# Kernel tuning notes

Measured on AMD Instinct MI355X. Metric: run time of the kernel, lower is better.

## Reference

```python
import jax, jax.numpy as jnp
import numpy as np

N_NODES = 100000
N_EDGES = 1600000
D_IN = 128
D_HID = 128
D_OUT = 40


def _linear_init(key, fan_in, fan_out):
    # torch nn.Linear default: U(-1/sqrt(fan_in), 1/sqrt(fan_in)) for W and b
    kw, kb = jax.random.split(key)
    bound = 1.0 / np.sqrt(fan_in)
    W = jax.random.uniform(kw, (fan_in, fan_out), jnp.float32, -bound, bound)
    b = jax.random.uniform(kb, (fan_out,), jnp.float32, -bound, bound)
    return W, b


def setup_inputs() -> dict:
    key = jax.random.key(0)
    ks = jax.random.split(key, 8)
    x = jax.random.normal(ks[0], (N_NODES, D_IN), jnp.float32)
    edges = jax.random.randint(ks[1], (2, N_EDGES), 0, N_NODES, jnp.int64)
    # layer 0: MLP(128 -> 128 -> 128)
    W1_0, b1_0 = _linear_init(ks[2], D_IN, D_HID)
    W2_0, b2_0 = _linear_init(ks[3], D_HID, D_HID)
    # layer 1: MLP(128 -> 128 -> 128)
    W1_1, b1_1 = _linear_init(ks[4], D_HID, D_HID)
    W2_1, b2_1 = _linear_init(ks[5], D_HID, D_HID)
    # layer 2: MLP(128 -> 128 -> 40)
    W1_2, b1_2 = _linear_init(ks[6], D_HID, D_HID)
    W2_2, b2_2 = _linear_init(ks[7], D_HID, D_OUT)
    eps = jnp.zeros(())  # GINConv train_eps=True initializes eps=0
    return {
        "x": x, "edges": edges,
        "W1_0": W1_0, "b1_0": b1_0, "W2_0": W2_0, "b2_0": b2_0, "eps_0": eps,
        "W1_1": W1_1, "b1_1": b1_1, "W2_1": W2_1, "b2_1": b2_1, "eps_1": eps,
        "W1_2": W1_2, "b1_2": b1_2, "W2_2": W2_2, "b2_2": b2_2, "eps_2": eps,
    }


def _gin_conv(x, src, dst, eps, W1, b1, W2, b2):
    # sum-aggregate neighbor features: out_i = MLP((1+eps)*x_i + sum_{j->i} x_j)
    aggr = jax.ops.segment_sum(x[src], dst, num_segments=x.shape[0])
    h = (1.0 + eps) * x + aggr
    h = jnp.maximum(h @ W1 + b1, 0.0)  # MLP layer 1 + ReLU
    return h @ W2 + b2                  # MLP layer 2


def reference(x, edges,
              W1_0, b1_0, W2_0, b2_0, eps_0,
              W1_1, b1_1, W2_1, b2_1, eps_1,
              W1_2, b1_2, W2_2, b2_2, eps_2):
    src, dst = edges[0], edges[1]
    # dropout is identity at inference (training=False)
    h = jax.nn.relu(_gin_conv(x, src, dst, eps_0, W1_0, b1_0, W2_0, b2_0))
    h = jax.nn.relu(_gin_conv(h, src, dst, eps_1, W1_1, b1_1, W2_1, b2_1))
    o = _gin_conv(h, src, dst, eps_2, W1_2, b1_2, W2_2, b2_2)
    return jax.nn.log_softmax(o, axis=1)
```

## Files before the change

kernel.cpp:

```cpp
#include <hip/hip_runtime.h>
#include <stdint.h>

typedef __attribute__((ext_vector_type(8))) short short8;
typedef __attribute__((ext_vector_type(4))) short short4v;
typedef __attribute__((ext_vector_type(4))) float float4v;

__device__ __forceinline__ float bf2f(unsigned short s) {
    union { unsigned int u; float f; } c; c.u = ((unsigned int)s) << 16; return c.f;
}
__device__ __forceinline__ unsigned short f2bf(float f) {
    union { float f; unsigned int u; } c; c.f = f;
    unsigned int x = c.u;
    unsigned int r = x + 0x7fffu + ((x >> 16) & 1u);
    return (unsigned short)(r >> 16);
}
__device__ __forceinline__ void unpack2(unsigned int u, float& lo, float& hi) {
    union { unsigned int uu; float ff; } a, b;
    a.uu = u << 16;
    b.uu = u & 0xffff0000u;
    lo = a.ff; hi = b.ff;
}

__global__ __launch_bounds__(256) void bs_count(const int* __restrict__ dst, int nE,
                                                int* __restrict__ bucketCnt) {
    __shared__ int c[512];
    int t = threadIdx.x;
    for (int i = t; i < 512; i += 256) c[i] = 0;
    __syncthreads();
    int base = blockIdx.x * 4096;
    for (int i = t; i < 4096; i += 256) {
        int e = base + i;
        if (e < nE) atomicAdd(&c[dst[e] >> 8], 1);
    }
    __syncthreads();
    for (int i = t; i < 512; i += 256)
        if (c[i]) atomicAdd(&bucketCnt[i], c[i]);
}

__global__ __launch_bounds__(512) void bs_scan(const int* __restrict__ bucketCnt,
                                               int* __restrict__ bucketBase,
                                               int* __restrict__ bucketCur,
                                               int* __restrict__ off, int M, int nE) {
    __shared__ int s[512];
    int t = threadIdx.x;
    int v = bucketCnt[t];
    s[t] = v;
    __syncthreads();
    for (int o = 1; o < 512; o <<= 1) {
        int x = (t >= o) ? s[t - o] : 0;
        __syncthreads();
        s[t] += x;
        __syncthreads();
    }
    bucketBase[t] = s[t] - v;
    bucketCur[t] = s[t] - v;
    if (t == 511) bucketBase[512] = s[511];
    if (t == 0) off[M] = nE;
}

__global__ __launch_bounds__(512) void bs_scatter(const int* __restrict__ src,
                                                  const int* __restrict__ dst, int nE,
                                                  int* __restrict__ bucketCur,
                                                  unsigned int* __restrict__ ebuf) {
    __shared__ int cnt[512];
    __shared__ int excl[512];
    __shared__ int chunk[512];
    __shared__ unsigned int buf[4096];
    __shared__ unsigned short bkt[4096];
    int t = threadIdx.x;
    cnt[t] = 0;
    __syncthreads();
    int base = blockIdx.x * 4096;
    int n = nE - base; if (n > 4096) n = 4096;
    unsigned int pk[8]; int bk[8]; int rk[8];
#pragma unroll
    for (int u = 0; u < 8; ++u) {
        int i = t + u * 512;
        if (i < n) {
            int e = base + i;
            int d = dst[e];
            int b = d >> 8;
            bk[u] = b;
            pk[u] = (unsigned int)src[e] | ((unsigned int)(d & 255) << 17);
            rk[u] = atomicAdd(&cnt[b], 1);
        } else bk[u] = -1;
    }
    __syncthreads();
    excl[t] = cnt[t];
    __syncthreads();
    for (int o = 1; o < 512; o <<= 1) {
        int x = (t >= o) ? excl[t - o] : 0;
        __syncthreads();
        excl[t] += x;
        __syncthreads();
    }
    int ex = excl[t] - cnt[t];
    __syncthreads();
    excl[t] = ex;
    if (cnt[t]) chunk[t] = atomicAdd(&bucketCur[t], cnt[t]);
    __syncthreads();
#pragma unroll
    for (int u = 0; u < 8; ++u) {
        if (bk[u] >= 0) {
            int lp = excl[bk[u]] + rk[u];
            buf[lp] = pk[u];
            bkt[lp] = (unsigned short)bk[u];
        }
    }
    __syncthreads();
    for (int i = t; i < n; i += 512) {
        int b = bkt[i];
        ebuf[chunk[b] + (i - excl[b])] = buf[i];
    }
}

__global__ __launch_bounds__(512) void bs_build(const unsigned int* __restrict__ ebuf,
                                                const int* __restrict__ bucketBase,
                                                int* __restrict__ off,
                                                int* __restrict__ esrc, int M) {
    __shared__ int cnt[256];
    __shared__ int excl[256];
    __shared__ int obuf[5120];
    int t = threadIdx.x, b = blockIdx.x;
    int base = bucketBase[b];
    int n = bucketBase[b + 1] - base;
    if (t < 256) cnt[t] = 0;
    __syncthreads();
    unsigned int pk[10]; int dl[10]; int rk[10];
#pragma unroll
    for (int u = 0; u < 10; ++u) {
        int i = t + u * 512;
        if (i < n) {
            unsigned int p = ebuf[base + i];
            pk[u] = p;
            int d = (p >> 17) & 255;
            dl[u] = d;
            rk[u] = atomicAdd(&cnt[d], 1);
        } else dl[u] = -1;
    }
    __syncthreads();
    if (t < 256) excl[t] = cnt[t];
    __syncthreads();
    for (int o = 1; o < 256; o <<= 1) {
        int x = (t < 256 && t >= o) ? excl[t - o] : 0;
        __syncthreads();
        if (t < 256) excl[t] += x;
        __syncthreads();
    }
    if (t < 256) {
        int ex = excl[t] - cnt[t];
        int node = b * 256 + t;
        if (node < M) off[node] = base + ex;
        excl[t] = ex;
    }
    __syncthreads();
#pragma unroll
    for (int u = 0; u < 10; ++u) {
        if (dl[u] >= 0) {
            int lp = excl[dl[u]] + rk[u];
            if (lp < 5120) obuf[lp] = (int)(pk[u] & 0x1FFFF);
        }
    }
    __syncthreads();
    for (int i = t; i < n; i += 512) esrc[base + i] = obuf[i];
}

struct Prep {
    const float* W[6];
    unsigned short* hi[6];
    const float4* xin;
    uint2* xout;
    int n4;
};

__global__ __launch_bounds__(256) void k_prep(Prep p) {
    int b = blockIdx.x;
    if (b < 344) {
        int mat = b >> 6;
        int rel = b - mat * 64;
        int NPAD = (mat == 5) ? 48 : 128;
        int N = (mat == 5) ? 40 : 128;
        int idx = rel * 256 + threadIdx.x;
        if (idx >= NPAD * 128) return;
        int n = idx >> 7, k = idx & 127;
        float w = (n < N) ? p.W[mat][k * N + n] : 0.f;
        p.hi[mat][idx] = f2bf(w);
    } else {
        int i = (b - 344) * 256 + threadIdx.x;
        if (i >= p.n4) return;
        float4 v = p.xin[i];
        uint2 o;
        o.x = ((unsigned int)f2bf(v.y) << 16) | f2bf(v.x);
        o.y = ((unsigned int)f2bf(v.w) << 16) | f2bf(v.z);
        p.xout[i] = o;
    }
}

__device__ __forceinline__ void acc8(uint4 v, float* s) {
    float a, b;
    unpack2(v.x, a, b); s[0] += a; s[1] += b;
    unpack2(v.y, a, b); s[2] += a; s[3] += b;
    unpack2(v.z, a, b); s[4] += a; s[5] += b;
    unpack2(v.w, a, b); s[6] += a; s[7] += b;
}

__global__ __launch_bounds__(256) void k_aggr(const uint4* __restrict__ Hin,
                                              const int* __restrict__ off,
                                              const int* __restrict__ esrc,
                                              const float* __restrict__ epsp,
                                              uint4* __restrict__ Ahi, int M) {
    int w = threadIdx.x >> 6, lane = threadIdx.x & 63;
    int li = lane & 15, q = lane >> 4;
    int node = blockIdx.x * 16 + w * 4 + q;
    if (node >= M) return;
    float ep = 1.0f + epsp[0];
    uint4 ow = Hin[node * 16 + li];
    float s[8] = {0.f, 0.f, 0.f, 0.f, 0.f, 0.f, 0.f, 0.f};
    int i = off[node], e = off[node + 1];
    for (; i + 8 <= e; i += 8) {
        uint4 v[8];
#pragma unroll
        for (int j = 0; j < 8; ++j) v[j] = Hin[esrc[i + j] * 16 + li];
#pragma unroll
        for (int j = 0; j < 8; ++j) acc8(v[j], s);
    }
    if (i < e) {
        int last = e - 1;
        uint4 v[8];
#pragma unroll
        for (int j = 0; j < 8; ++j) {
            int idx = i + j;
            int cl = idx < last ? idx : last;
            v[j] = Hin[esrc[cl] * 16 + li];
        }
#pragma unroll
        for (int j = 0; j < 8; ++j) {
            bool ok = (i + j) < e;
            uint4 u;
            u.x = ok ? v[j].x : 0u;
            u.y = ok ? v[j].y : 0u;
            u.z = ok ? v[j].z : 0u;
            u.w = ok ? v[j].w : 0u;
            acc8(u, s);
        }
    }
    float o[8];
    unpack2(ow.x, o[0], o[1]);
    unpack2(ow.y, o[2], o[3]);
    unpack2(ow.z, o[4], o[5]);
    unpack2(ow.w, o[6], o[7]);
#pragma unroll
    for (int k = 0; k < 8; ++k) s[k] = ep * o[k] + s[k];
    uint4 r;
    r.x = ((unsigned int)f2bf(s[1]) << 16) | f2bf(s[0]);
    r.y = ((unsigned int)f2bf(s[3]) << 16) | f2bf(s[2]);
    r.z = ((unsigned int)f2bf(s[5]) << 16) | f2bf(s[4]);
    r.w = ((unsigned int)f2bf(s[7]) << 16) | f2bf(s[6]);
    Ahi[node * 16 + li] = r;
}

template <int NT2, bool LOGITS>
__global__ __launch_bounds__(256, 4) void k_mlp(const unsigned short* __restrict__ AhiS,
                                                const unsigned short* __restrict__ W1h,
                                                const float* __restrict__ B1,
                                                const unsigned short* __restrict__ W2h,
                                                const float* __restrict__ B2,
                                                unsigned short* __restrict__ HOut,
                                                float* __restrict__ LOut, int M) {
    __shared__ short wbuf[128 * 136];
    int t = threadIdx.x, w = t >> 6, lane = t & 63;
    int lm = lane & 15, lg = lane >> 4;
    int rbase = blockIdx.x * 128;

    for (int i = t * 8; i < 128 * 128; i += 2048) {
        int n = i >> 7, k = i & 127;
        *(short8*)&wbuf[n * 136 + k] = *(const short8*)(W1h + i);
    }
    __syncthreads();

    short4v h2[2][8];
    bool act[2];
#pragma unroll
    for (int t2 = 0; t2 < 2; ++t2) {
        int r0 = rbase + t2 * 64 + w * 16;
        act[t2] = (r0 < M);
        if (act[t2]) {
            const short* Xp = (const short*)AhiS + (r0 + lm) * 128 + lg * 8;
            short8 xf[4];
#pragma unroll
            for (int kb = 0; kb < 4; ++kb) xf[kb] = *(const short8*)(Xp + kb * 32);
            float4v acc1[8];
#pragma unroll
            for (int nt = 0; nt < 8; ++nt) acc1[nt] = (float4v){0.f, 0.f, 0.f, 0.f};
#pragma unroll
            for (int nt = 0; nt < 8; ++nt) {
#pragma unroll
                for (int kb = 0; kb < 4; ++kb) {
                    short8 wf = *(const short8*)&wbuf[(nt * 16 + lm) * 136 + kb * 32 + lg * 8];
                    acc1[nt] = __builtin_amdgcn_mfma_f32_16x16x32_bf16(wf, xf[kb], acc1[nt], 0, 0, 0);
                }
            }
#pragma unroll
            for (int nt = 0; nt < 8; ++nt) {
                float4 b1 = *(const float4*)(B1 + nt * 16 + lg * 4);
                float v0 = acc1[nt][0] + b1.x; v0 = v0 > 0.f ? v0 : 0.f;
                float v1 = acc1[nt][1] + b1.y; v1 = v1 > 0.f ? v1 : 0.f;
                float v2 = acc1[nt][2] + b1.z; v2 = v2 > 0.f ? v2 : 0.f;
                float v3 = acc1[nt][3] + b1.w; v3 = v3 > 0.f ? v3 : 0.f;
                h2[t2][nt] = (short4v){(short)f2bf(v0), (short)f2bf(v1),
                                       (short)f2bf(v2), (short)f2bf(v3)};
            }
        } else {
#pragma unroll
            for (int nt = 0; nt < 8; ++nt) h2[t2][nt] = (short4v){0, 0, 0, 0};
        }
    }

    __syncthreads();
    for (int i = t * 8; i < NT2 * 16 * 128; i += 2048) {
        int n = i >> 7, k = i & 127;
        *(short8*)&wbuf[n * 136 + k] = *(const short8*)(W2h + i);
    }
    __syncthreads();

    float4v acc2[2][NT2];
#pragma unroll
    for (int t2 = 0; t2 < 2; ++t2)
#pragma unroll
        for (int ot = 0; ot < NT2; ++ot) acc2[t2][ot] = (float4v){0.f, 0.f, 0.f, 0.f};
#pragma unroll
    for (int ot = 0; ot < NT2; ++ot) {
#pragma unroll
        for (int nt = 0; nt < 8; ++nt) {
            short4v wf = *(const short4v*)&wbuf[(ot * 16 + lm) * 136 + nt * 16 + lg * 4];
#pragma unroll
            for (int t2 = 0; t2 < 2; ++t2)
                acc2[t2][ot] = __builtin_amdgcn_mfma_f32_16x16x16bf16_1k(wf, h2[t2][nt],
                                                                         acc2[t2][ot], 0, 0, 0);
        }
    }

#pragma unroll
    for (int t2 = 0; t2 < 2; ++t2) {
        if (!act[t2]) continue;
        int row = rbase + t2 * 64 + w * 16 + lm;
        if (!LOGITS) {
#pragma unroll
            for (int ot = 0; ot < NT2; ++ot) {
                float4 b2 = *(const float4*)(B2 + ot * 16 + lg * 4);
                float v0 = acc2[t2][ot][0] + b2.x; v0 = v0 > 0.f ? v0 : 0.f;
                float v1 = acc2[t2][ot][1] + b2.y; v1 = v1 > 0.f ? v1 : 0.f;
                float v2 = acc2[t2][ot][2] + b2.z; v2 = v2 > 0.f ? v2 : 0.f;
                float v3 = acc2[t2][ot][3] + b2.w; v3 = v3 > 0.f ? v3 : 0.f;
                uint2 pk;
                pk.x = ((unsigned int)f2bf(v1) << 16) | f2bf(v0);
                pk.y = ((unsigned int)f2bf(v3) << 16) | f2bf(v2);
                *(uint2*)(HOut + row * 128 + ot * 16 + lg * 4) = pk;
            }
        } else {
            float vv[NT2][4];
#pragma unroll
            for (int ot = 0; ot < NT2; ++ot) {
                int ub = ot * 16 + lg * 4;
                bool valid = ub <= 36;
                float4 b2 = valid ? *(const float4*)(B2 + ub) : (float4){0.f, 0.f, 0.f, 0.f};
                vv[ot][0] = valid ? acc2[t2][ot][0] + b2.x : -1e30f;
                vv[ot][1] = valid ? acc2[t2][ot][1] + b2.y : -1e30f;
                vv[ot][2] = valid ? acc2[t2][ot][2] + b2.z : -1e30f;
                vv[ot][3] = valid ? acc2[t2][ot][3] + b2.w : -1e30f;
            }
            float m = -1e30f;
#pragma unroll
            for (int ot = 0; ot < NT2; ++ot)
#pragma unroll
                for (int r = 0; r < 4; ++r) m = fmaxf(m, vv[ot][r]);
            m = fmaxf(m, __shfl_xor(m, 16, 64));
            m = fmaxf(m, __shfl_xor(m, 32, 64));
            float s = 0.f;
#pragma unroll
            for (int ot = 0; ot < NT2; ++ot)
#pragma unroll
                for (int r = 0; r < 4; ++r)
                    s += (vv[ot][r] > -1e29f) ? expf(vv[ot][r] - m) : 0.f;
            s += __shfl_xor(s, 16, 64);
            s += __shfl_xor(s, 32, 64);
            float ls = m + logf(s);
#pragma unroll
            for (int ot = 0; ot < NT2; ++ot) {
                int ub = ot * 16 + lg * 4;
                if (ub <= 36) {
                    float4 outv = {vv[ot][0] - ls, vv[ot][1] - ls,
                                   vv[ot][2] - ls, vv[ot][3] - ls};
                    *(float4*)(LOut + row * 40 + ub) = outv;
                }
            }
        }
    }
}

extern "C" void kernel_launch(void* const* d_in, const int* in_sizes, int n_in,
                              void* d_out, int out_size, void* d_ws, size_t ws_size,
                              hipStream_t stream) {
    const float* x    = (const float*)d_in[0];
    const int*   edges = (const int*)d_in[1];
    const float* eps0 = (const float*)d_in[6];
    const float* eps1 = (const float*)d_in[11];
    const float* eps2 = (const float*)d_in[16];
    const float* B1[3] = {(const float*)d_in[3], (const float*)d_in[8], (const float*)d_in[13]};
    const float* B2[3] = {(const float*)d_in[5], (const float*)d_in[10], (const float*)d_in[15]};

    int M  = in_sizes[0] / 128;
    int nE = in_sizes[1] / 2;
    const int* e_src = edges;
    const int* e_dst = edges + nE;

    char* ws = (char*)d_ws;
    size_t o = 0;
    auto alloc = [&](size_t bytes) {
        size_t p = o;
        o = (o + bytes + 511) & ~(size_t)511;
        return ws + p;
    };
    int* bucketCnt  = (int*)alloc(512 * 4);
    int* bucketBase = (int*)alloc(513 * 4);
    int* bucketCur  = (int*)alloc(512 * 4);
    int* off  = (int*)alloc((size_t)(M + 1) * 4);
    int* esrc = (int*)alloc((size_t)nE * 4);
    unsigned int* ebuf = (unsigned int*)alloc((size_t)nE * 4);

    Prep pp;
    pp.W[0] = (const float*)d_in[2];  pp.W[1] = (const float*)d_in[4];
    pp.W[2] = (const float*)d_in[7];  pp.W[3] = (const float*)d_in[9];
    pp.W[4] = (const float*)d_in[12]; pp.W[5] = (const float*)d_in[14];
    for (int m = 0; m < 6; ++m) {
        int npad = (m == 5) ? 48 : 128;
        pp.hi[m] = (unsigned short*)alloc((size_t)npad * 128 * 2);
    }
    unsigned short* xb  = (unsigned short*)alloc((size_t)M * 128 * 2);
    unsigned short* Ahi = (unsigned short*)alloc((size_t)M * 128 * 2);
    unsigned short* Hb  = (unsigned short*)alloc((size_t)M * 128 * 2);
    pp.xin = (const float4*)x;
    pp.xout = (uint2*)xb;
    pp.n4 = M * 32;
    (void)ws_size; (void)n_in; (void)out_size;

    hipMemsetAsync(bucketCnt, 0, 512 * 4, stream);
    int nChunk = (nE + 4095) / 4096;
    int nBk = (M + 255) / 256;
    bs_count<<<nChunk, 256, 0, stream>>>(e_dst, nE, bucketCnt);
    bs_scan<<<1, 512, 0, stream>>>(bucketCnt, bucketBase, bucketCur, off, M, nE);
    bs_scatter<<<nChunk, 512, 0, stream>>>(e_src, e_dst, nE, bucketCur, ebuf);
    bs_build<<<nBk, 512, 0, stream>>>(ebuf, bucketBase, off, esrc, M);
    k_prep<<<344 + (pp.n4 + 255) / 256, 256, 0, stream>>>(pp);

    int gA = (M + 15) / 16;
    int gG = (M + 127) / 128;

    k_aggr<<<gA, 256, 0, stream>>>((const uint4*)xb, off, esrc, eps0, (uint4*)Ahi, M);
    k_mlp<8, false><<<gG, 256, 0, stream>>>(Ahi, pp.hi[0], B1[0],
                                            pp.hi[1], B2[0], Hb, nullptr, M);
    k_aggr<<<gA, 256, 0, stream>>>((const uint4*)Hb, off, esrc, eps1, (uint4*)Ahi, M);
    k_mlp<8, false><<<gG, 256, 0, stream>>>(Ahi, pp.hi[2], B1[1],
                                            pp.hi[3], B2[1], Hb, nullptr, M);
    k_aggr<<<gA, 256, 0, stream>>>((const uint4*)Hb, off, esrc, eps2, (uint4*)Ahi, M);
    k_mlp<3, true><<<gG, 256, 0, stream>>>(Ahi, pp.hi[4], B1[2],
                                           pp.hi[5], B2[2], nullptr,
                                           (float*)d_out, M);
}
```

Baseline: 404.2 us.

## Fold memset into prep, split aggregation launches, prefetch MLP weights to registers

The bucket counter memset is moved into k_prep, which now runs first, so one launch is removed. Each aggregation pass is split into two launches over the two halves of the nodes. k_mlp now loads the activation tiles and both weight matrices into registers up front, then stages them into shared memory, and its occupancy bound drops from 4 to 2 blocks per CU. The changes aim to cut launch and memset overhead and hide global-load latency in the MLP, at the cost of more register pressure and extra aggregation launches.

```diff
diff --git a/kernel.cpp b/kernel.cpp
--- a/kernel.cpp
+++ b/kernel.cpp
@@ -171,10 +171,15 @@
     const float4* xin;
     uint2* xout;
     int n4;
+    int* bucketCnt;
 };
 
 __global__ __launch_bounds__(256) void k_prep(Prep p) {
     int b = blockIdx.x;
+    if (b == 0) {
+        p.bucketCnt[threadIdx.x] = 0;
+        p.bucketCnt[threadIdx.x + 256] = 0;
+    }
     if (b < 344) {
         int mat = b >> 6;
         int rel = b - mat * 64;
@@ -208,11 +213,12 @@
                                               const int* __restrict__ off,
                                               const int* __restrict__ esrc,
                                               const float* __restrict__ epsp,
-                                              uint4* __restrict__ Ahi, int M) {
+                                              uint4* __restrict__ Ahi,
+                                              int base, int limit) {
     int w = threadIdx.x >> 6, lane = threadIdx.x & 63;
     int li = lane & 15, q = lane >> 4;
-    int node = blockIdx.x * 16 + w * 4 + q;
-    if (node >= M) return;
+    int node = base + blockIdx.x * 16 + w * 4 + q;
+    if (node >= limit) return;
     float ep = 1.0f + epsp[0];
     uint4 ow = Hin[node * 16 + li];
     float s[8] = {0.f, 0.f, 0.f, 0.f, 0.f, 0.f, 0.f, 0.f};
@@ -260,7 +266,7 @@
 }
 
 template <int NT2, bool LOGITS>
-__global__ __launch_bounds__(256, 4) void k_mlp(const unsigned short* __restrict__ AhiS,
+__global__ __launch_bounds__(256, 2) void k_mlp(const unsigned short* __restrict__ AhiS,
                                                 const unsigned short* __restrict__ W1h,
                                                 const float* __restrict__ B1,
                                                 const unsigned short* __restrict__ W2h,
@@ -272,13 +278,7 @@
     int lm = lane & 15, lg = lane >> 4;
     int rbase = blockIdx.x * 128;
 
-    for (int i = t * 8; i < 128 * 128; i += 2048) {
-        int n = i >> 7, k = i & 127;
-        *(short8*)&wbuf[n * 136 + k] = *(const short8*)(W1h + i);
-    }
-    __syncthreads();
-
-    short4v h2[2][8];
+    short8 xf2[2][4];
     bool act[2];
 #pragma unroll
     for (int t2 = 0; t2 < 2; ++t2) {
@@ -286,40 +286,58 @@
         act[t2] = (r0 < M);
         if (act[t2]) {
             const short* Xp = (const short*)AhiS + (r0 + lm) * 128 + lg * 8;
-            short8 xf[4];
-#pragma unroll
-            for (int kb = 0; kb < 4; ++kb) xf[kb] = *(const short8*)(Xp + kb * 32);
-            float4v acc1[8];
-#pragma unroll
-            for (int nt = 0; nt < 8; ++nt) acc1[nt] = (float4v){0.f, 0.f, 0.f, 0.f};
-#pragma unroll
-            for (int nt = 0; nt < 8; ++nt) {
-#pragma unroll
-                for (int kb = 0; kb < 4; ++kb) {
-                    short8 wf = *(const short8*)&wbuf[(nt * 16 + lm) * 136 + kb * 32 + lg * 8];
-                    acc1[nt] = __builtin_amdgcn_mfma_f32_16x16x32_bf16(wf, xf[kb], acc1[nt], 0, 0, 0);
-                }
+#pragma unroll
+            for (int kb = 0; kb < 4; ++kb) xf2[t2][kb] = *(const short8*)(Xp + kb * 32);
+        } else {
+#pragma unroll
+            for (int kb = 0; kb < 4; ++kb) xf2[t2][kb] = (short8){0,0,0,0,0,0,0,0};
+        }
+    }
+    constexpr int W2CH = (NT2 * 16 * 128) / 2048;
+    short8 w1r[8], w2r[W2CH];
+#pragma unroll
+    for (int u = 0; u < 8; ++u) w1r[u] = *(const short8*)(W1h + t * 8 + u * 2048);
+#pragma unroll
+    for (int u = 0; u < W2CH; ++u) w2r[u] = *(const short8*)(W2h + t * 8 + u * 2048);
+
+#pragma unroll
+    for (int u = 0; u < 8; ++u) {
+        int i = t * 8 + u * 2048;
+        *(short8*)&wbuf[(i >> 7) * 136 + (i & 127)] = w1r[u];
+    }
+    __syncthreads();
+
+    short4v h2[2][8];
+#pragma unroll
+    for (int t2 = 0; t2 < 2; ++t2) {
+        float4v acc1[8];
+#pragma unroll
+        for (int nt = 0; nt < 8; ++nt) acc1[nt] = (float4v){0.f, 0.f, 0.f, 0.f};
+#pragma unroll
+        for (int nt = 0; nt < 8; ++nt) {
+#pragma unroll
+            for (int kb = 0; kb < 4; ++kb) {
+                short8 wf = *(const short8*)&wbuf[(nt * 16 + lm) * 136 + kb * 32 + lg * 8];
+                acc1[nt] = __builtin_amdgcn_mfma_f32_16x16x32_bf16(wf, xf2[t2][kb], acc1[nt], 0, 0, 0);
             }
-#pragma unroll
-            for (int nt = 0; nt < 8; ++nt) {
-                float4 b1 = *(const float4*)(B1 + nt * 16 + lg * 4);
-                float v0 = acc1[nt][0] + b1.x; v0 = v0 > 0.f ? v0 : 0.f;
-                float v1 = acc1[nt][1] + b1.y; v1 = v1 > 0.f ? v1 : 0.f;
-                float v2 = acc1[nt][2] + b1.z; v2 = v2 > 0.f ? v2 : 0.f;
-                float v3 = acc1[nt][3] + b1.w; v3 = v3 > 0.f ? v3 : 0.f;
-                h2[t2][nt] = (short4v){(short)f2bf(v0), (short)f2bf(v1),
-                                       (short)f2bf(v2), (short)f2bf(v3)};
-            }
-        } else {
-#pragma unroll
-            for (int nt = 0; nt < 8; ++nt) h2[t2][nt] = (short4v){0, 0, 0, 0};
-        }
-    }
-
-    __syncthreads();
-    for (int i = t * 8; i < NT2 * 16 * 128; i += 2048) {
-        int n = i >> 7, k = i & 127;
-        *(short8*)&wbuf[n * 136 + k] = *(const short8*)(W2h + i);
+        }
+#pragma unroll
+        for (int nt = 0; nt < 8; ++nt) {
+            float4 b1 = *(const float4*)(B1 + nt * 16 + lg * 4);
+            float v0 = acc1[nt][0] + b1.x; v0 = v0 > 0.f ? v0 : 0.f;
+            float v1 = acc1[nt][1] + b1.y; v1 = v1 > 0.f ? v1 : 0.f;
+            float v2 = acc1[nt][2] + b1.z; v2 = v2 > 0.f ? v2 : 0.f;
+            float v3 = acc1[nt][3] + b1.w; v3 = v3 > 0.f ? v3 : 0.f;
+            h2[t2][nt] = (short4v){(short)f2bf(v0), (short)f2bf(v1),
+                                   (short)f2bf(v2), (short)f2bf(v3)};
+        }
+    }
+
+    __syncthreads();
+#pragma unroll
+    for (int u = 0; u < W2CH; ++u) {
+        int i = t * 8 + u * 2048;
+        *(short8*)&wbuf[(i >> 7) * 136 + (i & 127)] = w2r[u];
     }
     __syncthreads();
 
@@ -442,27 +460,32 @@
     pp.xin = (const float4*)x;
     pp.xout = (uint2*)xb;
     pp.n4 = M * 32;
+    pp.bucketCnt = bucketCnt;
     (void)ws_size; (void)n_in; (void)out_size;
 
-    hipMemsetAsync(bucketCnt, 0, 512 * 4, stream);
     int nChunk = (nE + 4095) / 4096;
     int nBk = (M + 255) / 256;
+    k_prep<<<344 + (pp.n4 + 255) / 256, 256, 0, stream>>>(pp);
     bs_count<<<nChunk, 256, 0, stream>>>(e_dst, nE, bucketCnt);
     bs_scan<<<1, 512, 0, stream>>>(bucketCnt, bucketBase, bucketCur, off, M, nE);
     bs_scatter<<<nChunk, 512, 0, stream>>>(e_src, e_dst, nE, bucketCur, ebuf);
     bs_build<<<nBk, 512, 0, stream>>>(ebuf, bucketBase, off, esrc, M);
-    k_prep<<<344 + (pp.n4 + 255) / 256, 256, 0, stream>>>(pp);
-
-    int gA = (M + 15) / 16;
+
+    int h0 = ((M / 2) + 15) & ~15;
+    int gA0 = (h0 + 15) / 16;
+    int gA1 = (M - h0 + 15) / 16;
     int gG = (M + 127) / 128;
 
-    k_aggr<<<gA, 256, 0, stream>>>((const uint4*)xb, off, esrc, eps0, (uint4*)Ahi, M);
+    k_aggr<<<gA0, 256, 0, stream>>>((const uint4*)xb, off, esrc, eps0, (uint4*)Ahi, 0, h0);
+    k_aggr<<<gA1, 256, 0, stream>>>((const uint4*)xb, off, esrc, eps0, (uint4*)Ahi, h0, M);
     k_mlp<8, false><<<gG, 256, 0, stream>>>(Ahi, pp.hi[0], B1[0],
                                             pp.hi[1], B2[0], Hb, nullptr, M);
-    k_aggr<<<gA, 256, 0, stream>>>((const uint4*)Hb, off, esrc, eps1, (uint4*)Ahi, M);
+    k_aggr<<<gA0, 256, 0, stream>>>((const uint4*)Hb, off, esrc, eps1, (uint4*)Ahi, 0, h0);
+    k_aggr<<<gA1, 256, 0, stream>>>((const uint4*)Hb, off, esrc, eps1, (uint4*)Ahi, h0, M);
     k_mlp<8, false><<<gG, 256, 0, stream>>>(Ahi, pp.hi[2], B1[1],
                                             pp.hi[3], B2[1], Hb, nullptr, M);
-    k_aggr<<<gA, 256, 0, stream>>>((const uint4*)Hb, off, esrc, eps2, (uint4*)Ahi, M);
+    k_aggr<<<gA0, 256, 0, stream>>>((const uint4*)Hb, off, esrc, eps2, (uint4*)Ahi, 0, h0);
+    k_aggr<<<gA1, 256, 0, stream>>>((const uint4*)Hb, off, esrc, eps2, (uint4*)Ahi, h0, M);
     k_mlp<3, true><<<gG, 256, 0, stream>>>(Ahi, pp.hi[4], B1[2],
                                            pp.hi[5], B2[2], nullptr,
                                            (float*)d_out, M);
```

Result: slower. 415.9 us (+2.9%).
